# Performance work log

Measured on AMD Instinct MI355X. Metric: run time of the kernel, lower is better.

The kernel has to match this reference:

```python
import jax, jax.numpy as jnp
import numpy as np

B, IMG, P, D, E, K, H = 32, 224, 16, 512, 8, 2, 8
G = IMG // P
T = G * G          # 196 patches
PD = P * P         # 256 patch dim
FF = 4 * D         # expert hidden

def _posenc(t, d):
    pos = jnp.arange(t, dtype=jnp.float32)[:, None]
    i = jnp.arange(0, d, 2, dtype=jnp.float32)
    ang = pos / jnp.power(10000.0, i / d)
    pe = jnp.zeros((t, d), jnp.float32)
    pe = pe.at[:, 0::2].set(jnp.sin(ang))
    pe = pe.at[:, 1::2].set(jnp.cos(ang))
    return pe

def _attn(x, Wq, Wk, Wv, Wo, bo):
    bs, t, d = x.shape
    hs = d // H
    q = (x @ Wq).reshape(bs, t, H, hs).transpose(0, 2, 1, 3)
    k = (x @ Wk).reshape(bs, t, H, hs).transpose(0, 2, 1, 3)
    v = (x @ Wv).reshape(bs, t, H, hs).transpose(0, 2, 1, 3)
    wei = jnp.einsum('bhqd,bhkd->bhqk', q, k) * (hs ** -0.5)
    mask = jnp.tril(jnp.ones((t, t), dtype=bool))
    wei = jax.nn.softmax(jnp.where(mask, wei, -jnp.inf), axis=-1)
    o = jnp.einsum('bhqk,bhkd->bhqd', wei, v).transpose(0, 2, 1, 3).reshape(bs, t, d)
    return o @ Wo + bo

def _router(x, Wt, bt, Wn, bn, noise):
    # NoisyTopkRouter: noisy logits, top-k scatter to -inf background, softmax
    logits = x @ Wt + bt
    noisy = logits + noise * jax.nn.softplus(x @ Wn + bn)
    _, topi = jax.lax.top_k(noisy, K)
    sel = jax.nn.one_hot(topi, E, dtype=jnp.float32).sum(-2) > 0  # [B,T,E] bool
    return jax.nn.softmax(jnp.where(sel, noisy, -jnp.inf), axis=-1)

def _moe(x, gate, Wi, bi, Wo, bo):
    # gate is exactly zero off the top-k set, so dense all-expert compute
    # weighted by gate equals the original masked gather/scatter-add combine.
    h = jax.nn.relu(jnp.einsum('btd,edh->bteh', x, Wi) + bi)
    y = jnp.einsum('bteh,ehd->bted', h, Wo) + bo
    return jnp.einsum('bte,bted->btd', gate, y)

def _ln(x, g, b):
    mu = x.mean(-1, keepdims=True)
    var = ((x - mu) ** 2).mean(-1, keepdims=True)
    return (x - mu) / jnp.sqrt(var + 1e-5) * g + b

def _moe_layer(x, pW, pb, Wq, Wk, Wv, Wo, bo, rtW, rtb, rnW, rnb, eWi, ebi, eWo, ebo, lng, lnb, noise):
    x = x @ pW + pb                       # input_projection
    x = _attn(x, Wq, Wk, Wv, Wo, bo)      # multi-head causal self-attention
    gate = _router(x, rtW, rtb, rnW, rnb, noise)
    y = _moe(x, gate, eWi, ebi, eWo, ebo)
    return _ln(y, lng, lnb)               # dropout is identity in eval

def setup_inputs():
    key = jax.random.key(0)
    shapes = {"x": (B, 1, IMG, IMG), "pemb_W": (PD, D), "pemb_b": (D,), "vec_W": (D, D), "vec_b": (D,), "cls_W": (D, D), "cls_b": (D,)}
    for l in ("1", "2"):
        shapes.update({f"p{l}_W": (D, D), f"p{l}_b": (D,), f"Wq{l}": (D, D), f"Wk{l}": (D, D), f"Wv{l}": (D, D), f"Wo{l}": (D, D), f"bo{l}": (D,), f"rt{l}_W": (D, E), f"rt{l}_b": (E,), f"rn{l}_W": (D, E), f"rn{l}_b": (E,), f"eWi{l}": (E, D, FF), f"ebi{l}": (E, FF), f"eWo{l}": (E, FF, D), f"ebo{l}": (E, D), f"ln{l}_g": (D,), f"ln{l}_b": (D,), f"noise{l}": (B, T, E)})
    out = {}
    for i, (name, shp) in enumerate(shapes.items()):
        k = jax.random.fold_in(key, i)
        if name.startswith("ln") and name.endswith("_g"):
            out[name] = jnp.ones(shp, jnp.float32)
        else:
            scale = 1.0 if name == "x" or name.startswith("noise") else 0.02
            out[name] = jax.random.normal(k, shp, jnp.float32) * scale
    return out

def reference(x, pemb_W, pemb_b, vec_W, vec_b, cls_W, cls_b, p1_W, p1_b, Wq1, Wk1, Wv1, Wo1, bo1, rt1_W, rt1_b, rn1_W, rn1_b, eWi1, ebi1, eWo1, ebo1, ln1_g, ln1_b, noise1, p2_W, p2_b, Wq2, Wk2, Wv2, Wo2, bo2, rt2_W, rt2_b, rn2_W, rn2_b, eWi2, ebi2, eWo2, ebo2, ln2_g, ln2_b, noise2):
    bs = x.shape[0]
    # patchify (c==1): [B,1,IMG,IMG] -> [B,T,PD]
    patches = x[:, 0].reshape(bs, G, P, G, P).transpose(0, 1, 3, 2, 4).reshape(bs, T, PD)
    h = patches @ pemb_W + pemb_b + _posenc(T, D)[None]
    f1 = _moe_layer(h, p1_W, p1_b, Wq1, Wk1, Wv1, Wo1, bo1, rt1_W, rt1_b, rn1_W, rn1_b, eWi1, ebi1, eWo1, ebo1, ln1_g, ln1_b, noise1)
    first_vector = f1 @ vec_W + vec_b
    f2 = _moe_layer(first_vector, p2_W, p2_b, Wq2, Wk2, Wv2, Wo2, bo2, rt2_W, rt2_b, rn2_W, rn2_b, eWi2, ebi2, eWo2, ebo2, ln2_g, ln2_b, noise2)
    second_vector = f2 @ vec_W + vec_b
    # source bug: second_attn_weights is None; treated as uniform ones ->
    # mean over dim1 of ones is 1, so global = sum over patches.
    global_vector = second_vector.sum(axis=1)
    cls_vector = global_vector @ cls_W + cls_b
    return first_vector, second_vector, global_vector, cls_vector
```

## Files before the change

kernel.cpp:

```cpp
#include <hip/hip_runtime.h>

#define BT 6272
#define TT 196
#define DM 512
#define FFD 2048
#define NE 8
#define ABUF 3211264
#define SLOTS 12544

typedef float f32x4 __attribute__((ext_vector_type(4)));
typedef __bf16 bf16x8 __attribute__((ext_vector_type(8)));

__device__ __forceinline__ ushort f2bf(float f){
  union { float f; unsigned u; } v; v.f = f;
  unsigned u = v.u;
  u += 0x7fffu + ((u >> 16) & 1u);
  return (ushort)(u >> 16);
}
__device__ __forceinline__ float bf2f(ushort u){
  union { unsigned u; float f; } c; c.u = ((unsigned)u) << 16; return c.f;
}
__device__ __forceinline__ void splitbf(float v, ushort& hi, ushort& lo){
  union { float f; unsigned u; } c; c.f = v;
  hi = (ushort)(c.u >> 16);
  union { unsigned u; float f; } hf; hf.u = c.u & 0xffff0000u;
  lo = f2bf(v - hf.f);
}
__device__ __forceinline__ void glds16(const ushort* g, ushort* l){
  __builtin_amdgcn_global_load_lds(
      (const __attribute__((address_space(1))) unsigned int*)g,
      (__attribute__((address_space(3))) unsigned int*)l, 16, 0, 0);
}
__device__ __forceinline__ int xcd_swz(int f, int nwg){
  int q = nwg >> 3, r = nwg & 7;
  int xcd = f & 7, i = f >> 3;
  return (xcd < r ? xcd*(q+1) : r*(q+1) + (xcd-r)*q) + i;
}

__global__ void patchify_k(const float* __restrict__ x, ushort* __restrict__ oh, ushort* __restrict__ ol){
  int bt = blockIdx.x;
  int t = bt % TT, b = bt / TT;
  int pd = threadIdx.x;
  int g1 = t / 14, g2 = t % 14, p1 = pd >> 4, p2 = pd & 15;
  int src = (b*224 + g1*16 + p1)*224 + g2*16 + p2;
  float v = x[src];
  ushort hu, lu; splitbf(v, hu, lu);
  oh[(size_t)bt*256 + pd] = hu;
  ol[(size_t)bt*256 + pd] = lu;
}

__global__ void posenc_k(float* __restrict__ pe){
  int t = blockIdx.x, c = threadIdx.x;
  int m2 = c & ~1;
  double ang = (double)t * pow(10000.0, -(double)m2 / 512.0);
  double vv = (c & 1) ? cos(ang) : sin(ang);
  pe[t*DM + c] = (float)vv;
}

__global__ __launch_bounds__(256)
void wsplit_k(const float* __restrict__ src, ushort* __restrict__ dh, ushort* __restrict__ dl,
              int R, int C){
  __shared__ float t[32][33];
  int c0 = blockIdx.x << 5, r0 = blockIdx.y << 5;
  int tx = threadIdx.x & 31, ty = threadIdx.x >> 5;
  #pragma unroll
  for (int i = 0; i < 32; i += 8)
    t[ty+i][tx] = src[(size_t)(r0+ty+i)*C + c0 + tx];
  __syncthreads();
  #pragma unroll
  for (int i = 0; i < 32; i += 8){
    float v = t[tx][ty+i];
    ushort hu, lu; splitbf(v, hu, lu);
    dh[(size_t)(c0+ty+i)*R + r0 + tx] = hu;
    dl[(size_t)(c0+ty+i)*R + r0 + tx] = lu;
  }
}

__global__ __launch_bounds__(256)
void wsplit5e_k(const float* __restrict__ s0, const float* __restrict__ s1,
                const float* __restrict__ s2, const float* __restrict__ s3,
                const float* __restrict__ s4,
                ushort* __restrict__ dQkvH, ushort* __restrict__ dQkvL,
                ushort* __restrict__ dWoH, ushort* __restrict__ dWoL,
                ushort* __restrict__ dPWh, ushort* __restrict__ dPWl)
{
  int z = blockIdx.z;
  int c0 = blockIdx.x << 5, r0 = blockIdx.y << 5;
  int tx = threadIdx.x & 31, ty = threadIdx.x >> 5;
  if (z == 4){
    #pragma unroll
    for (int i = 0; i < 32; i += 8){
      size_t idx = (size_t)(r0+ty+i)*DM + c0 + tx;
      ushort hu, lu; splitbf(s4[idx], hu, lu);
      dPWh[idx] = hu; dPWl[idx] = lu;
    }
    return;
  }
  const float* src = (z==0)? s0 : (z==1)? s1 : (z==2)? s2 : s3;
  ushort* dh; ushort* dl;
  if (z == 3){ dh = dWoH; dl = dWoL; }
  else { dh = dQkvH + (size_t)z*DM*DM; dl = dQkvL + (size_t)z*DM*DM; }
  __shared__ float t[32][33];
  #pragma unroll
  for (int i = 0; i < 32; i += 8)
    t[ty+i][tx] = src[(size_t)(r0+ty+i)*DM + c0 + tx];
  __syncthreads();
  #pragma unroll
  for (int i = 0; i < 32; i += 8){
    float v = t[tx][ty+i];
    ushort hu, lu; splitbf(v, hu, lu);
    dh[(size_t)(c0+ty+i)*DM + r0 + tx] = hu;
    dl[(size_t)(c0+ty+i)*DM + r0 + tx] = lu;
  }
}

__global__ __launch_bounds__(256)
void bfold_k(const float* __restrict__ pb, const float* __restrict__ Wq,
             const float* __restrict__ Wk, const float* __restrict__ Wv,
             float* __restrict__ bf){
  int tid = threadIdx.x;
  int w = tid >> 6, lane = tid & 63;
  int n = blockIdx.x*4 + w;
  const float* W = (n < 512) ? Wq : (n < 1024) ? Wk : Wv;
  int c = n & 511;
  float s = 0.f;
  #pragma unroll
  for (int u = 0; u < 8; ++u){
    int d = (u<<6) + lane;
    s += pb[d] * W[(size_t)d*DM + c];
  }
  #pragma unroll
  for (int off = 32; off; off >>= 1) s += __shfl_xor(s, off, 64);
  if (lane == 0) bf[n] = s;
}

__global__ __launch_bounds__(256)
void gemm_s(const ushort* __restrict__ Ah, const ushort* __restrict__ Al,
            const ushort* __restrict__ Bh, const ushort* __restrict__ Bl,
            const float* __restrict__ bias, const float* __restrict__ pe,
            float* __restrict__ Cf, ushort* __restrict__ Ch, ushort* __restrict__ Cl,
            int N, int kld)
{
  __shared__ __align__(16) ushort smem[4][2*128*32];
  ushort* Ahs = smem[0];
  ushort* Als = smem[1];
  ushort* Bhs = smem[2];
  ushort* Bls = smem[3];
  int gx = gridDim.x, gy = gridDim.y;
  int fblk = blockIdx.x + gx*blockIdx.y;
  int wgt = xcd_swz(fblk, gx*gy);
  int bx = wgt % gx, by = wgt / gx;
  int row0 = by << 7, col0 = bx << 7;
  int tid = threadIdx.x;
  int lane = tid & 63, w = tid >> 6;
  int wr = w >> 1, wc = w & 1;
  int fr = lane & 15, fu = lane >> 4;
  int srow = 16*w + (lane >> 2);
  int cs = ((lane & 3) ^ ((srow >> 1) & 3)) << 3;
  const ushort* gAh0 = Ah + (size_t)(row0 + srow) * kld + cs;
  const ushort* gAh1 = Ah + (size_t)(row0 + 64 + srow) * kld + cs;
  const ushort* gAl0 = Al + (size_t)(row0 + srow) * kld + cs;
  const ushort* gAl1 = Al + (size_t)(row0 + 64 + srow) * kld + cs;
  const ushort* gBh0 = Bh + (size_t)(col0 + srow) * kld + cs;
  const ushort* gBh1 = Bh + (size_t)(col0 + 64 + srow) * kld + cs;
  const ushort* gBl0 = Bl + (size_t)(col0 + srow) * kld + cs;
  const ushort* gBl1 = Bl + (size_t)(col0 + 64 + srow) * kld + cs;
  int lo0 = (16*w)*32, lo1 = (64+16*w)*32;
  #define GSTAGE(koff, nb) { \
    glds16(gAh0 + (koff), &Ahs[(nb)+lo0]); glds16(gAh1 + (koff), &Ahs[(nb)+lo1]); \
    glds16(gAl0 + (koff), &Als[(nb)+lo0]); glds16(gAl1 + (koff), &Als[(nb)+lo1]); \
    glds16(gBh0 + (koff), &Bhs[(nb)+lo0]); glds16(gBh1 + (koff), &Bhs[(nb)+lo1]); \
    glds16(gBl0 + (koff), &Bls[(nb)+lo0]); glds16(gBl1 + (koff), &Bls[(nb)+lo1]); }
  f32x4 acc[4][4] = {};
  int nt = kld >> 5;
  GSTAGE(0, 0)
  GSTAGE(32, 128*32)
  for (int t = 0; t < nt; ++t){
    if (t + 1 < nt) asm volatile("s_waitcnt vmcnt(8)" ::: "memory");
    else            asm volatile("s_waitcnt vmcnt(0)" ::: "memory");
    __builtin_amdgcn_s_barrier();
    asm volatile("" ::: "memory");
    int cb = (t & 1) * (128*32);
    bf16x8 ah[4], al[4];
    #pragma unroll
    for (int i = 0; i < 4; ++i){
      int Ra = (wr<<6) + (i<<4) + fr;
      int oa = cb + Ra*32 + ((fu ^ ((Ra>>1)&3))<<3);
      ah[i] = *(const bf16x8*)&Ahs[oa];
      al[i] = *(const bf16x8*)&Als[oa];
    }
    #pragma unroll
    for (int j = 0; j < 4; ++j){
      int Rb = (wc<<6) + (j<<4) + fr;
      int ob = cb + Rb*32 + ((fu ^ ((Rb>>1)&3))<<3);
      bf16x8 bh = *(const bf16x8*)&Bhs[ob];
      bf16x8 bl = *(const bf16x8*)&Bls[ob];
      #pragma unroll
      for (int i = 0; i < 4; ++i){
        acc[i][j] = __builtin_amdgcn_mfma_f32_16x16x32_bf16(ah[i], bh, acc[i][j], 0, 0, 0);
        acc[i][j] = __builtin_amdgcn_mfma_f32_16x16x32_bf16(al[i], bh, acc[i][j], 0, 0, 0);
        acc[i][j] = __builtin_amdgcn_mfma_f32_16x16x32_bf16(ah[i], bl, acc[i][j], 0, 0, 0);
      }
    }
    asm volatile("" ::: "memory");
    __builtin_amdgcn_s_barrier();
    if (t + 2 < nt) GSTAGE((t+2) << 5, (t & 1) * (128*32))
  }
  #undef GSTAGE
  int fq = lane >> 4;
  if (Cf){
    #pragma unroll
    for (int j = 0; j < 4; ++j){
      int col = col0 + (wc<<6) + (j<<4) + fr;
      float bv = bias ? bias[col] : 0.f;
      #pragma unroll
      for (int i = 0; i < 4; ++i){
        #pragma unroll
        for (int q = 0; q < 4; ++q){
          int rr = row0 + (wr<<6) + (i<<4) + (fq<<2) + q;
          float v = acc[i][j][q] + bv;
          if (pe) v += pe[(size_t)(rr % TT)*DM + col];
          Cf[(size_t)rr*N + col] = v;
        }
      }
    }
  }
  if (Ch){
    ushort* Lh = smem[0];
    ushort* Ll = smem[2];
    __syncthreads();
    #pragma unroll
    for (int j = 0; j < 4; ++j){
      int lcol = (wc<<6) + (j<<4) + fr;
      int col = col0 + lcol;
      float bv = bias ? bias[col] : 0.f;
      #pragma unroll
      for (int i = 0; i < 4; ++i){
        #pragma unroll
        for (int q = 0; q < 4; ++q){
          int lrow = (wr<<6) + (i<<4) + (fq<<2) + q;
          float v = acc[i][j][q] + bv;
          if (pe) v += pe[(size_t)((row0 + lrow) % TT)*DM + col];
          ushort hu, lu; splitbf(v, hu, lu);
          int g = (lrow >> 2) & 7;
          int idx = lrow*128 + ((((lcol>>3) ^ g))<<3) + (lcol & 7);
          Lh[idx] = hu; Ll[idx] = lu;
        }
      }
    }
    __syncthreads();
    #pragma unroll
    for (int pass = 0; pass < 8; ++pass){
      int lrow = pass*16 + (tid >> 4);
      int s = tid & 15;
      int g = (lrow >> 2) & 7;
      int idx = lrow*128 + ((s ^ g)<<3);
      uint4 vh = *(const uint4*)&Lh[idx];
      uint4 vl = *(const uint4*)&Ll[idx];
      size_t off = (size_t)(row0 + lrow)*N + col0 + s*8;
      *(uint4*)&Ch[off] = vh;
      *(uint4*)&Cl[off] = vl;
    }
  }
}

__global__ __launch_bounds__(256)
void gemm_f32(const float* __restrict__ A, const float* __restrict__ Bw,
              float* __restrict__ C, const float* __restrict__ bias,
              float* __restrict__ obf, int M, int N, int K)
{
  __shared__ float As[16][68];
  __shared__ float Bs[16][68];
  int tid = threadIdx.x;
  int row0 = blockIdx.y << 6, col0 = blockIdx.x << 6;
  int ar = tid >> 2, ak = (tid & 3) << 2;
  int bk = tid >> 4, bn = (tid & 15) << 2;
  int n0 = (tid & 15) << 2, m0 = (tid >> 4) << 2;
  float acc[4][4] = {};
  bool arow_ok = (row0 + ar) < M;
  const float* Aldg = A + (size_t)(row0 + ar) * K + ak;
  const float* Bldg = Bw + (size_t)bk * N + col0 + bn;
  for (int k0 = 0; k0 < K; k0 += 16){
    float4 av = make_float4(0.f,0.f,0.f,0.f);
    if (arow_ok) av = *(const float4*)(Aldg + k0);
    float4 bv = *(const float4*)(Bldg + (size_t)k0 * N);
    __syncthreads();
    As[ak+0][ar]=av.x; As[ak+1][ar]=av.y; As[ak+2][ar]=av.z; As[ak+3][ar]=av.w;
    *(float4*)&Bs[bk][bn] = bv;
    __syncthreads();
    #pragma unroll
    for (int kk = 0; kk < 16; ++kk){
      float4 a = *(const float4*)&As[kk][m0];
      float4 b = *(const float4*)&Bs[kk][n0];
      float aa[4] = {a.x,a.y,a.z,a.w};
      float bb[4] = {b.x,b.y,b.z,b.w};
      #pragma unroll
      for (int i = 0; i < 4; ++i)
        #pragma unroll
        for (int j = 0; j < 4; ++j)
          acc[i][j] += aa[i]*bb[j];
    }
  }
  float4 badd = make_float4(0.f,0.f,0.f,0.f);
  if (bias) badd = *(const float4*)(bias + col0 + n0);
  #pragma unroll
  for (int i = 0; i < 4; ++i){
    int gr = row0 + m0 + i;
    if (gr < M){
      float4 r = make_float4(acc[i][0]+badd.x, acc[i][1]+badd.y, acc[i][2]+badd.z, acc[i][3]+badd.w);
      *(float4*)(C + (size_t)gr*N + col0 + n0) = r;
      if (obf) *(float4*)(obf + (size_t)gr*N + col0 + n0) = r;
    }
  }
}

__global__ __launch_bounds__(256)
void fattn_k(const ushort* __restrict__ Xh, const ushort* __restrict__ Xl,
             ushort* __restrict__ oh, ushort* __restrict__ ol)
{
  __shared__ ushort Kh[64][72], Kl[64][72];
  __shared__ ushort Vth[64][72], Vtl[64][72];
  __shared__ ushort Ph[64][72], Pl[64][72];
  int qt = blockIdx.x, bh = blockIdx.y;
  int b = bh >> 3, h = bh & 7;
  int tid = threadIdx.x;
  int w = tid >> 6, lane = tid & 63;
  int fr = lane & 15, fu = lane >> 4;
  int qrow_f = qt*64 + w*16 + fr;
  int qtok = b*TT + (qrow_f < TT ? qrow_f : TT-1);
  const ushort* qph = Xh + (size_t)qtok*1536 + h*64 + fu*8;
  const ushort* qpl = Xl + (size_t)qtok*1536 + h*64 + fu*8;
  bf16x8 qh0 = *(const bf16x8*)(qph);
  bf16x8 qh1 = *(const bf16x8*)(qph + 32);
  bf16x8 ql0 = *(const bf16x8*)(qpl);
  bf16x8 ql1 = *(const bf16x8*)(qpl + 32);
  f32x4 o_acc[4] = {};
  float m_i[4], l_i[4];
  #pragma unroll
  for (int q = 0; q < 4; ++q){ m_i[q] = -3e38f; l_i[q] = 0.f; }
  int sr = tid >> 2, sc = (tid & 3) << 4;
  int ktiles = qt + 1;
  for (int kt = 0; kt < ktiles; ++kt){
    __syncthreads();
    {
      int jrow = kt*64 + sr;
      int jtok = b*TT + (jrow < TT ? jrow : TT-1);
      const ushort* kph = Xh + (size_t)jtok*1536 + 512 + h*64 + sc;
      const ushort* kpl = Xl + (size_t)jtok*1536 + 512 + h*64 + sc;
      *(uint4*)&Kh[sr][sc]   = *(const uint4*)kph;
      *(uint4*)&Kh[sr][sc+8] = *(const uint4*)(kph + 8);
      *(uint4*)&Kl[sr][sc]   = *(const uint4*)kpl;
      *(uint4*)&Kl[sr][sc+8] = *(const uint4*)(kpl + 8);
      const ushort* vph = Xh + (size_t)jtok*1536 + 1024 + h*64 + sc;
      const ushort* vpl = Xl + (size_t)jtok*1536 + 1024 + h*64 + sc;
      ushort tv[16];
      *(uint4*)&tv[0] = *(const uint4*)vph;
      *(uint4*)&tv[8] = *(const uint4*)(vph + 8);
      #pragma unroll
      for (int t = 0; t < 16; ++t) Vth[sc + t][sr] = tv[t];
      *(uint4*)&tv[0] = *(const uint4*)vpl;
      *(uint4*)&tv[8] = *(const uint4*)(vpl + 8);
      #pragma unroll
      for (int t = 0; t < 16; ++t) Vtl[sc + t][sr] = tv[t];
    }
    __syncthreads();
    f32x4 sacc[4] = {};
    #pragma unroll
    for (int j = 0; j < 4; ++j){
      bf16x8 kh0 = *(const bf16x8*)&Kh[j*16 + fr][fu*8];
      bf16x8 kh1 = *(const bf16x8*)&Kh[j*16 + fr][32 + fu*8];
      bf16x8 kl0 = *(const bf16x8*)&Kl[j*16 + fr][fu*8];
      bf16x8 kl1 = *(const bf16x8*)&Kl[j*16 + fr][32 + fu*8];
      sacc[j] = __builtin_amdgcn_mfma_f32_16x16x32_bf16(qh0, kh0, sacc[j], 0, 0, 0);
      sacc[j] = __builtin_amdgcn_mfma_f32_16x16x32_bf16(ql0, kh0, sacc[j], 0, 0, 0);
      sacc[j] = __builtin_amdgcn_mfma_f32_16x16x32_bf16(qh0, kl0, sacc[j], 0, 0, 0);
      sacc[j] = __builtin_amdgcn_mfma_f32_16x16x32_bf16(qh1, kh1, sacc[j], 0, 0, 0);
      sacc[j] = __builtin_amdgcn_mfma_f32_16x16x32_bf16(ql1, kh1, sacc[j], 0, 0, 0);
      sacc[j] = __builtin_amdgcn_mfma_f32_16x16x32_bf16(qh1, kl1, sacc[j], 0, 0, 0);
    }
    int rbase = qt*64 + w*16 + (fu<<2);
    int cg = kt*64 + fr;
    float p[4][4];
    #pragma unroll
    for (int q = 0; q < 4; ++q){
      int rg = rbase + q;
      float sv[4];
      #pragma unroll
      for (int j = 0; j < 4; ++j){
        int cj = cg + j*16;
        sv[j] = (cj <= rg && cj < TT) ? sacc[j][q]*0.125f : -3e38f;
      }
      float mx = fmaxf(fmaxf(sv[0],sv[1]), fmaxf(sv[2],sv[3]));
      #pragma unroll
      for (int off = 1; off < 16; off <<= 1) mx = fmaxf(mx, __shfl_xor(mx, off, 64));
      float mnew = fmaxf(m_i[q], mx);
      float al = expf(m_i[q] - mnew);
      l_i[q] *= al;
      o_acc[0][q] *= al; o_acc[1][q] *= al; o_acc[2][q] *= al; o_acc[3][q] *= al;
      float ps = 0.f;
      #pragma unroll
      for (int j = 0; j < 4; ++j){ p[q][j] = expf(sv[j] - mnew); ps += p[q][j]; }
      #pragma unroll
      for (int off = 1; off < 16; off <<= 1) ps += __shfl_xor(ps, off, 64);
      l_i[q] += ps;
      m_i[q] = mnew;
    }
    #pragma unroll
    for (int q = 0; q < 4; ++q){
      int pr = w*16 + (fu<<2) + q;
      #pragma unroll
      for (int j = 0; j < 4; ++j){
        ushort hu, lu; splitbf(p[q][j], hu, lu);
        Ph[pr][j*16 + fr] = hu;
        Pl[pr][j*16 + fr] = lu;
      }
    }
    bf16x8 ph0 = *(const bf16x8*)&Ph[w*16 + fr][fu*8];
    bf16x8 ph1 = *(const bf16x8*)&Ph[w*16 + fr][32 + fu*8];
    bf16x8 pl0 = *(const bf16x8*)&Pl[w*16 + fr][fu*8];
    bf16x8 pl1 = *(const bf16x8*)&Pl[w*16 + fr][32 + fu*8];
    #pragma unroll
    for (int jd = 0; jd < 4; ++jd){
      bf16x8 vh0 = *(const bf16x8*)&Vth[jd*16 + fr][fu*8];
      bf16x8 vh1 = *(const bf16x8*)&Vth[jd*16 + fr][32 + fu*8];
      bf16x8 vl0 = *(const bf16x8*)&Vtl[jd*16 + fr][fu*8];
      bf16x8 vl1 = *(const bf16x8*)&Vtl[jd*16 + fr][32 + fu*8];
      o_acc[jd] = __builtin_amdgcn_mfma_f32_16x16x32_bf16(ph0, vh0, o_acc[jd], 0, 0, 0);
      o_acc[jd] = __builtin_amdgcn_mfma_f32_16x16x32_bf16(pl0, vh0, o_acc[jd], 0, 0, 0);
      o_acc[jd] = __builtin_amdgcn_mfma_f32_16x16x32_bf16(ph0, vl0, o_acc[jd], 0, 0, 0);
      o_acc[jd] = __builtin_amdgcn_mfma_f32_16x16x32_bf16(ph1, vh1, o_acc[jd], 0, 0, 0);
      o_acc[jd] = __builtin_amdgcn_mfma_f32_16x16x32_bf16(pl1, vh1, o_acc[jd], 0, 0, 0);
      o_acc[jd] = __builtin_amdgcn_mfma_f32_16x16x32_bf16(ph1, vl1, o_acc[jd], 0, 0, 0);
    }
  }
  #pragma unroll
  for (int q = 0; q < 4; ++q){
    int rg = qt*64 + w*16 + (fu<<2) + q;
    if (rg < TT){
      float inv = 1.f / l_i[q];
      size_t rowoff = (size_t)(b*TT + rg)*DM + h*64 + fr;
      #pragma unroll
      for (int jd = 0; jd < 4; ++jd){
        float v = o_acc[jd][q] * inv;
        ushort hu, lu; splitbf(v, hu, lu);
        oh[rowoff + jd*16] = hu;
        ol[rowoff + jd*16] = lu;
      }
    }
  }
}

__global__ __launch_bounds__(256)
void router2_k(const ushort* __restrict__ Xh, const ushort* __restrict__ Xl,
               const float* __restrict__ rtW, const float* __restrict__ rtb,
               const float* __restrict__ rnW, const float* __restrict__ rnb, const float* __restrict__ nz,
               int* __restrict__ tok_e, float* __restrict__ tok_g)
{
  __shared__ float Wt[8*513];
  __shared__ float Wn[8*513];
  int tid = threadIdx.x;
  for (int i = tid*4; i < DM*8; i += 1024){
    float4 t = *(const float4*)(rtW + i);
    float4 n = *(const float4*)(rnW + i);
    int d = i >> 3, e = i & 7;
    Wt[(e+0)*513 + d] = t.x; Wt[(e+1)*513 + d] = t.y; Wt[(e+2)*513 + d] = t.z; Wt[(e+3)*513 + d] = t.w;
    Wn[(e+0)*513 + d] = n.x; Wn[(e+1)*513 + d] = n.y; Wn[(e+2)*513 + d] = n.z; Wn[(e+3)*513 + d] = n.w;
  }
  __syncthreads();
  int w = tid >> 6, lane = tid & 63;
  int t = (blockIdx.x << 2) + w;
  const ushort* xh = Xh + (size_t)t * DM;
  const ushort* xl = Xl + (size_t)t * DM;
  float at[8] = {}, an[8] = {};
  #pragma unroll
  for (int u = 0; u < 8; ++u){
    int d = (u<<6) + lane;
    float xv = bf2f(xh[d]) + bf2f(xl[d]);
    #pragma unroll
    for (int e = 0; e < 8; ++e){
      at[e] += xv * Wt[e*513 + d];
      an[e] += xv * Wn[e*513 + d];
    }
  }
  #pragma unroll
  for (int off = 32; off; off >>= 1){
    #pragma unroll
    for (int e = 0; e < 8; ++e){
      at[e] += __shfl_xor(at[e], off, 64);
      an[e] += __shfl_xor(an[e], off, 64);
    }
  }
  if (lane == 0){
    float ns[8];
    #pragma unroll
    for (int e = 0; e < 8; ++e){
      float lt = at[e] + rtb[e];
      float ln_ = an[e] + rnb[e];
      float sp = (ln_ > 0.f) ? (ln_ + log1pf(expf(-ln_))) : log1pf(expf(ln_));
      ns[e] = lt + nz[(size_t)t*8 + e] * sp;
    }
    int i1 = 0; float n1 = ns[0];
    #pragma unroll
    for (int e = 1; e < 8; ++e) if (ns[e] > n1){ n1 = ns[e]; i1 = e; }
    int i2 = -1; float n2 = -3e38f;
    #pragma unroll
    for (int e = 0; e < 8; ++e) if (e != i1 && ns[e] > n2){ n2 = ns[e]; i2 = e; }
    float ex = expf(n2 - n1);
    float inv = 1.f / (1.f + ex);
    tok_e[t*2]   = i1; tok_g[t*2]   = inv;
    tok_e[t*2+1] = i2; tok_g[t*2+1] = ex * inv;
  }
}

__global__ __launch_bounds__(1024)
void route_assign_k(const int* __restrict__ tok_e, int* __restrict__ offs_g,
                    int* __restrict__ idx_c, int* __restrict__ tok_slot)
{
  __shared__ int hist[NE];
  __shared__ int cur[NE];
  int tid = threadIdx.x;
  int lane = tid & 63;
  if (tid < NE) hist[tid] = 0;
  __syncthreads();
  for (int i = tid; i < BT*2; i += 1024){
    int e = tok_e[i];
    #pragma unroll
    for (int x = 0; x < NE; ++x){
      unsigned long long m = __ballot(e == x);
      if (m && lane == (int)__builtin_ctzll(m)) atomicAdd(&hist[x], __popcll(m));
    }
  }
  __syncthreads();
  if (tid == 0){
    int s = 0;
    for (int e = 0; e < NE; ++e){ offs_g[e] = s; cur[e] = s; s += hist[e]; }
    offs_g[NE] = s;
  }
  __syncthreads();
  for (int i = tid; i < BT*2; i += 1024){
    int e = tok_e[i];
    int p = 0;
    #pragma unroll
    for (int x = 0; x < NE; ++x){
      unsigned long long m = __ballot(e == x);
      if (m){
        int leader = (int)__builtin_ctzll(m);
        int bw = 0;
        if (lane == leader) bw = atomicAdd(&cur[x], __popcll(m));
        bw = __shfl(bw, leader, 64);
        if (e == x) p = bw + __popcll(m & ((lane == 63) ? 0x7fffffffffffffffull : ((1ull << lane) - 1ull)));
      }
    }
    idx_c[p] = i >> 1;
    tok_slot[i] = p;
  }
}

__global__ __launch_bounds__(256)
void transconv2_k(const float* __restrict__ eWi, const float* __restrict__ eWo,
                  ushort* __restrict__ WiT, ushort* __restrict__ WoT){
  __shared__ float t[32][33];
  int z = blockIdx.z;
  const float* src; ushort* dst; int R, C, c0, r0;
  if (z < NE){
    src = eWi + (size_t)z*DM*FFD; dst = WiT + (size_t)z*DM*FFD;
    R = DM; C = FFD; c0 = blockIdx.x << 5; r0 = blockIdx.y << 5;
  } else {
    int e = z - NE;
    src = eWo + (size_t)e*FFD*DM; dst = WoT + (size_t)e*FFD*DM;
    R = FFD; C = DM; c0 = blockIdx.y << 5; r0 = blockIdx.x << 5;
  }
  int tx = threadIdx.x & 31, ty = threadIdx.x >> 5;
  #pragma unroll
  for (int i = 0; i < 32; i += 8)
    t[ty+i][tx] = src[(size_t)(r0+ty+i)*C + c0 + tx];
  __syncthreads();
  #pragma unroll
  for (int i = 0; i < 32; i += 8)
    dst[(size_t)(c0+ty+i)*R + r0 + tx] = f2bf(t[tx][ty+i]);
}

template<int MODE>
__global__ __launch_bounds__(256)
void moe_mfma(const ushort* __restrict__ A, const int* __restrict__ aidx,
              const ushort* __restrict__ Bt,
              const float* __restrict__ bias, const int* __restrict__ offs,
              void* __restrict__ Out, int kld, int ldb, int out_ld, int accum)
{
  __shared__ __align__(16) ushort smem[2][2*128*32];
  ushort* As = smem[0];
  ushort* Bs = smem[1];
  int gx = gridDim.x, gy = gridDim.y;
  int nwg = gx * gy * (int)gridDim.z;
  int fblk = blockIdx.x + gx*(blockIdx.y + gy*blockIdx.z);
  int wgt = xcd_swz(fblk, nwg);
  int bx = wgt % gx; wgt /= gx;
  int by = wgt % gy; int bz = wgt / gy;
  int e = bz;
  int base = offs[e], cnt = offs[e+1] - base;
  int row0 = by << 7;
  if (row0 >= cnt) return;
  int col0 = bx << 7;
  int tid = threadIdx.x, lane = tid & 63, w = tid >> 6;
  int wr = w >> 1, wc = w & 1;
  int fr = lane & 15, fu = lane >> 4;
  int srow = 16*w + (lane >> 2);
  int cs = ((lane & 3) ^ ((srow >> 1) & 3)) << 3;
  int s0 = base + row0 + srow;      if (s0 > SLOTS-1) s0 = SLOTS-1;
  int s1 = base + row0 + 64 + srow; if (s1 > SLOTS-1) s1 = SLOTS-1;
  int r0i = (MODE == 0) ? aidx[s0] : s0;
  int r1i = (MODE == 0) ? aidx[s1] : s1;
  const ushort* gA0 = A + (size_t)r0i * kld + cs;
  const ushort* gA1 = A + (size_t)r1i * kld + cs;
  const ushort* Bb = Bt + (size_t)e * ((size_t)FFD*DM);
  const ushort* gB0 = Bb + (size_t)(col0 + srow) * ldb + cs;
  const ushort* gB1 = Bb + (size_t)(col0 + 64 + srow) * ldb + cs;
  int lo0 = (16*w)*32, lo1 = (64+16*w)*32;
  #define MSTAGE(koff, nb) { \
    glds16(gA0 + (koff), &As[(nb)+lo0]); glds16(gA1 + (koff), &As[(nb)+lo1]); \
    glds16(gB0 + (koff), &Bs[(nb)+lo0]); glds16(gB1 + (koff), &Bs[(nb)+lo1]); }
  f32x4 acc[4][4] = {};
  int nt = kld >> 5;
  MSTAGE(0, 0)
  MSTAGE(32, 128*32)
  for (int t = 0; t < nt; ++t){
    if (t + 1 < nt) asm volatile("s_waitcnt vmcnt(4)" ::: "memory");
    else            asm volatile("s_waitcnt vmcnt(0)" ::: "memory");
    __builtin_amdgcn_s_barrier();
    asm volatile("" ::: "memory");
    int cb = (t & 1) * (128*32);
    bf16x8 af[4], bf[4];
    #pragma unroll
    for (int i = 0; i < 4; ++i){
      int Ra = (wr<<6) + (i<<4) + fr;
      af[i] = *(const bf16x8*)&As[cb + Ra*32 + ((fu ^ ((Ra>>1)&3))<<3)];
      int Rb = (wc<<6) + (i<<4) + fr;
      bf[i] = *(const bf16x8*)&Bs[cb + Rb*32 + ((fu ^ ((Rb>>1)&3))<<3)];
    }
    #pragma unroll
    for (int i = 0; i < 4; ++i)
      #pragma unroll
      for (int j = 0; j < 4; ++j)
        acc[i][j] = __builtin_amdgcn_mfma_f32_16x16x32_bf16(af[i], bf[j], acc[i][j], 0, 0, 0);
    asm volatile("" ::: "memory");
    __builtin_amdgcn_s_barrier();
    if (t + 2 < nt) MSTAGE((t+2) << 5, (t & 1) * (128*32))
  }
  #undef MSTAGE
  int fq = lane >> 4;
  if (MODE == 0){
    ushort* Ls = smem[0];
    __syncthreads();
    #pragma unroll
    for (int j = 0; j < 4; ++j){
      int lcol = (wc<<6) + (j<<4) + fr;
      float bv = bias[(size_t)e*FFD + col0 + lcol];
      #pragma unroll
      for (int i = 0; i < 4; ++i){
        #pragma unroll
        for (int q = 0; q < 4; ++q){
          int lrow = (wr<<6) + (i<<4) + (fq<<2) + q;
          float vv = acc[i][j][q] + bv;
          int g = (lrow >> 2) & 7;
          Ls[lrow*128 + ((((lcol>>3) ^ g))<<3) + (lcol & 7)] = f2bf(fmaxf(vv, 0.f));
        }
      }
    }
    __syncthreads();
    #pragma unroll
    for (int pass = 0; pass < 8; ++pass){
      int lrow = pass*16 + (tid >> 4);
      int s = tid & 15;
      int g = (lrow >> 2) & 7;
      uint4 v = *(const uint4*)&Ls[lrow*128 + ((s ^ g)<<3)];
      int gr = row0 + lrow;
      if (gr < cnt)
        *(uint4*)&((ushort*)Out)[(size_t)(base+gr)*out_ld + col0 + s*8] = v;
    }
  } else {
    #pragma unroll
    for (int j = 0; j < 4; ++j){
      int col = col0 + (wc<<6) + (j<<4) + fr;
      float bv = bias[(size_t)e*DM + col];
      #pragma unroll
      for (int i = 0; i < 4; ++i){
        #pragma unroll
        for (int q = 0; q < 4; ++q){
          int rr = row0 + (wr<<6) + (i<<4) + (fq<<2) + q;
          if (rr < cnt){
            float* yp = (float*)Out + (size_t)(base+rr)*out_ld + col;
            *yp = acc[i][j][q] + (accum ? *yp : bv);
          }
        }
      }
    }
  }
}

__global__ __launch_bounds__(256)
void combine_ln_k(const float* __restrict__ Ye, const int* __restrict__ tok_slot,
                  const float* __restrict__ tok_g, const float* __restrict__ g,
                  const float* __restrict__ bb, ushort* __restrict__ oh, ushort* __restrict__ ol)
{
  int t = blockIdx.x, tid = threadIdx.x;
  int s1 = tok_slot[t*2], s2 = tok_slot[t*2+1];
  float g1 = tok_g[t*2], g2 = tok_g[t*2+1];
  const float* y1 = Ye + (size_t)s1*DM;
  const float* y2 = Ye + (size_t)s2*DM;
  float v0 = g1*y1[tid]     + g2*y2[tid];
  float v1 = g1*y1[tid+256] + g2*y2[tid+256];
  __shared__ float red[8];
  int w = tid >> 6, lane = tid & 63;
  float s = v0 + v1;
  #pragma unroll
  for (int off = 32; off; off >>= 1) s += __shfl_xor(s, off, 64);
  if (lane == 0) red[w] = s;
  __syncthreads();
  float mu = (red[0]+red[1]+red[2]+red[3]) * (1.f/512.f);
  float d0 = v0 - mu, d1 = v1 - mu;
  float q2 = d0*d0 + d1*d1;
  #pragma unroll
  for (int off = 32; off; off >>= 1) q2 += __shfl_xor(q2, off, 64);
  if (lane == 0) red[4+w] = q2;
  __syncthreads();
  float var = (red[4]+red[5]+red[6]+red[7]) * (1.f/512.f);
  float r = 1.f / sqrtf(var + 1e-5f);
  float r0v = d0*r*g[tid]     + bb[tid];
  float r1v = d1*r*g[tid+256] + bb[tid+256];
  ushort hu, lu;
  splitbf(r0v, hu, lu);
  oh[(size_t)t*DM + tid] = hu; ol[(size_t)t*DM + tid] = lu;
  splitbf(r1v, hu, lu);
  oh[(size_t)t*DM + tid + 256] = hu; ol[(size_t)t*DM + tid + 256] = lu;
}

__global__ void gsum_k(const float* __restrict__ sv, float* __restrict__ gb, float* __restrict__ gout){
  int i = blockIdx.x*256 + threadIdx.x;
  int b = i >> 9, d = i & 511;
  const float* p = sv + (size_t)b*TT*DM + d;
  float s = 0.f;
  for (int t = 0; t < TT; ++t) s += p[(size_t)t*DM];
  gb[i] = s; gout[i] = s;
}

extern "C" void kernel_launch(void* const* d_in, const int* in_sizes, int n_in,
                              void* d_out, int out_size, void* d_ws, size_t ws_size,
                              hipStream_t stream)
{
  (void)in_sizes; (void)n_in; (void)out_size;
  const float* xin   = (const float*)d_in[0];
  const float* pembW = (const float*)d_in[1];
  const float* pembB = (const float*)d_in[2];
  const float* vecW  = (const float*)d_in[3];
  const float* vecB  = (const float*)d_in[4];
  const float* clsW  = (const float*)d_in[5];
  const float* clsB  = (const float*)d_in[6];
  float* out = (float*)d_out;

  const size_t QKV_SH  = (size_t)2*BT*1536;
  const size_t RMIN_SH = QKV_SH + (size_t)2*1536*DM + (size_t)2*DM*DM;
  const size_t FIXF =
      (size_t)SLOTS*DM
    + (size_t)2*ABUF
    + (size_t)NE*FFD*DM
    + (size_t)256*DM
    + (size_t)DM*DM
    + (size_t)3*DM*DM
    + (size_t)DM*DM
    + (size_t)TT*DM + 2048
    + 16384*2 + SLOTS + SLOTS*3 + 64;
  int fcw = 256;
  for (int cand = 2048; cand >= 256; cand >>= 1){
    size_t reg_sh = (size_t)SLOTS*cand > RMIN_SH ? (size_t)SLOTS*cand : RMIN_SH;
    size_t need = (FIXF + reg_sh/2) * sizeof(float);
    if (need <= ws_size){ fcw = cand; break; }
  }
  size_t region_sh = (size_t)SLOTS*fcw > RMIN_SH ? (size_t)SLOTS*fcw : RMIN_SH;

  float* ws = (float*)d_ws;
  float* Yexp = ws;
  ushort* S0h = (ushort*)(Yexp + (size_t)SLOTS*DM);
  ushort* S0l = S0h + ABUF;
  ushort* S1h = S0l + ABUF;
  ushort* S1l = S1h + ABUF;
  ushort* region = S1l + ABUF;
  ushort* WiT  = region + region_sh;
  ushort* WoT  = WiT + (size_t)NE*FFD*DM;
  ushort* PembH = WoT + (size_t)NE*FFD*DM;
  ushort* PembL = PembH + 256*DM;
  ushort* VecH = PembL + 256*DM;
  ushort* VecL = VecH + DM*DM;
  ushort* QkvWH = VecL + DM*DM;
  ushort* QkvWL = QkvWH + 3*DM*DM;
  ushort* WoSH = QkvWL + 3*DM*DM;
  ushort* WoSL = WoSH + DM*DM;
  float* pe    = (float*)(WoSL + DM*DM);
  float* bfold = pe + TT*DM;
  float* gbv   = bfold + 2048;
  float* clsbuf= gbv + 16384;
  float* tok_g = clsbuf + 16384;
  int* tok_e   = (int*)(tok_g + SLOTS);
  int* tok_slot= tok_e + SLOTS;
  int* idx_c   = tok_slot + SLOTS;
  int* offs    = idx_c + SLOTS;
  ushort* QKVh = region;
  ushort* QKVl = region + (size_t)BT*1536;
  ushort* FoldWH = region + QKV_SH;
  ushort* FoldWL = FoldWH + (size_t)1536*DM;
  ushort* PWh  = FoldWL + (size_t)1536*DM;
  ushort* PWl  = PWh + (size_t)DM*DM;
  ushort* H1b  = region;
  ushort* PATh = region;
  ushort* PATl = region + (size_t)BT*256;

  patchify_k<<<dim3(BT), dim3(256), 0, stream>>>(xin, PATh, PATl);
  posenc_k<<<dim3(TT), dim3(512), 0, stream>>>(pe);
  wsplit_k<<<dim3(16, 8), dim3(256), 0, stream>>>(pembW, PembH, PembL, 256, DM);
  wsplit_k<<<dim3(16, 16), dim3(256), 0, stream>>>(vecW, VecH, VecL, DM, DM);
  gemm_s<<<dim3(4,49), dim3(256), 0, stream>>>(PATh, PATl, PembH, PembL, pembB, pe,
                                               nullptr, S0h, S0l, DM, 256);

  ushort *INh = S0h, *INl = S0l, *TPh = S1h, *TPl = S1l;
  for (int l = 0; l < 2; ++l){
    int base = 7 + 18*l;
    const float* pW  = (const float*)d_in[base+0];
    const float* pb  = (const float*)d_in[base+1];
    const float* Wq  = (const float*)d_in[base+2];
    const float* Wk  = (const float*)d_in[base+3];
    const float* Wv  = (const float*)d_in[base+4];
    const float* Wo  = (const float*)d_in[base+5];
    const float* bo  = (const float*)d_in[base+6];
    const float* rtW = (const float*)d_in[base+7];
    const float* rtb = (const float*)d_in[base+8];
    const float* rnW = (const float*)d_in[base+9];
    const float* rnb = (const float*)d_in[base+10];
    const float* eWi = (const float*)d_in[base+11];
    const float* ebi = (const float*)d_in[base+12];
    const float* eWo = (const float*)d_in[base+13];
    const float* ebo = (const float*)d_in[base+14];
    const float* lng = (const float*)d_in[base+15];
    const float* lnb = (const float*)d_in[base+16];
    const float* nz  = (const float*)d_in[base+17];

    wsplit5e_k<<<dim3(16,16,5), dim3(256), 0, stream>>>(Wq, Wk, Wv, Wo, pW,
                                                        QkvWH, QkvWL, WoSH, WoSL, PWh, PWl);
    gemm_s<<<dim3(4,12), dim3(256), 0, stream>>>(QkvWH, QkvWL, PWh, PWl, nullptr, nullptr,
                                                 nullptr, FoldWH, FoldWL, DM, DM);
    bfold_k<<<dim3(384), dim3(256), 0, stream>>>(pb, Wq, Wk, Wv, bfold);
    gemm_s<<<dim3(12,49), dim3(256), 0, stream>>>(INh, INl, FoldWH, FoldWL, bfold, nullptr,
                                                 nullptr, QKVh, QKVl, 1536, DM);
    fattn_k<<<dim3(4,256), dim3(256), 0, stream>>>(QKVh, QKVl, INh, INl);
    gemm_s<<<dim3(4,49), dim3(256), 0, stream>>>(INh, INl, WoSH, WoSL, bo, nullptr,
                                                 nullptr, TPh, TPl, DM, DM);
    transconv2_k<<<dim3(64, 16, 2*NE), dim3(256), 0, stream>>>(eWi, eWo, WiT, WoT);
    router2_k<<<dim3(BT/4), dim3(256), 0, stream>>>(TPh, TPl, rtW, rtb, rnW, rnb, nz, tok_e, tok_g);
    route_assign_k<<<dim3(1), dim3(1024), 0, stream>>>(tok_e, offs, idx_c, tok_slot);
    for (int c0 = 0; c0 < FFD; c0 += fcw){
      moe_mfma<0><<<dim3(fcw/128, 49, NE), dim3(256), 0, stream>>>(
          TPh, idx_c, WiT + (size_t)c0*DM, ebi + c0, offs, (void*)H1b, DM, DM, fcw, 0);
      moe_mfma<1><<<dim3(DM/128, 49, NE), dim3(256), 0, stream>>>(
          H1b, nullptr, WoT + c0, ebo, offs, (void*)Yexp, fcw, FFD, DM, c0);
    }
    combine_ln_k<<<dim3(BT), dim3(256), 0, stream>>>(Yexp, tok_slot, tok_g, lng, lnb, INh, INl);
    gemm_s<<<dim3(4,49), dim3(256), 0, stream>>>(INh, INl, VecH, VecL, vecB, nullptr,
                                                 out + (size_t)l*ABUF, TPh, TPl, DM, DM);
    ushort* th = INh; INh = TPh; TPh = th;
    ushort* tl = INl; INl = TPl; TPl = tl;
  }

  gsum_k<<<dim3(64), dim3(256), 0, stream>>>(out + ABUF, gbv, out + 2*ABUF);
  gemm_f32<<<dim3(8,1), dim3(256), 0, stream>>>(gbv, clsW, clsbuf, clsB, out + 2*ABUF + 16384, 32, DM, DM);
}
```

Before: 942.4 us.

## Compact MoE tile grid via tile map and triple-buffer GEMM K-loop

The routing kernel now builds a compact list of (expert, row-block) tiles, so the expert GEMMs launch over at most 112 row tiles instead of 49×8 mostly-empty blocks that would exit early. Empty launch slots cost less and the XCD swizzle spreads only real tiles. The MFMA K-loop moves from two LDS buffers to three, and the next stage is issued right after the barrier, which removes the second barrier per iteration. This triples A/B LDS use per block (48KB), which may lower occupancy.

```diff
diff --git a/kernel.cpp b/kernel.cpp
--- a/kernel.cpp
+++ b/kernel.cpp
@@ -7,6 +7,7 @@
 #define NE 8
 #define ABUF 3211264
 #define SLOTS 12544
+#define MAXTILES 112
 
 typedef float f32x4 __attribute__((ext_vector_type(4)));
 typedef __bf16 bf16x8 __attribute__((ext_vector_type(8)));
@@ -514,7 +515,8 @@
 
 __global__ __launch_bounds__(1024)
 void route_assign_k(const int* __restrict__ tok_e, int* __restrict__ offs_g,
-                    int* __restrict__ idx_c, int* __restrict__ tok_slot)
+                    int* __restrict__ idx_c, int* __restrict__ tok_slot,
+                    int* __restrict__ tmap)
 {
   __shared__ int hist[NE];
   __shared__ int cur[NE];
@@ -535,6 +537,12 @@
     int s = 0;
     for (int e = 0; e < NE; ++e){ offs_g[e] = s; cur[e] = s; s += hist[e]; }
     offs_g[NE] = s;
+    int tt = 0;
+    for (int e = 0; e < NE; ++e){
+      int nb = (hist[e] + 127) >> 7;
+      for (int b = 0; b < nb; ++b) tmap[tt++] = (e << 16) | b;
+    }
+    for (; tt < MAXTILES; ++tt) tmap[tt] = -1;
   }
   __syncthreads();
   for (int i = tid; i < BT*2; i += 1024){
@@ -585,21 +593,22 @@
 void moe_mfma(const ushort* __restrict__ A, const int* __restrict__ aidx,
               const ushort* __restrict__ Bt,
               const float* __restrict__ bias, const int* __restrict__ offs,
+              const int* __restrict__ tmap,
               void* __restrict__ Out, int kld, int ldb, int out_ld, int accum)
 {
-  __shared__ __align__(16) ushort smem[2][2*128*32];
-  ushort* As = smem[0];
-  ushort* Bs = smem[1];
+  __shared__ __align__(16) ushort smem[6*128*32];
+  const int TB = 128*32;
+  ushort* As = smem;
+  ushort* Bs = smem + 3*TB;
   int gx = gridDim.x, gy = gridDim.y;
-  int nwg = gx * gy * (int)gridDim.z;
-  int fblk = blockIdx.x + gx*(blockIdx.y + gy*blockIdx.z);
-  int wgt = xcd_swz(fblk, nwg);
-  int bx = wgt % gx; wgt /= gx;
-  int by = wgt % gy; int bz = wgt / gy;
-  int e = bz;
+  int fblk = blockIdx.x + gx*blockIdx.y;
+  int wgt = xcd_swz(fblk, gx*gy);
+  int bx = wgt % gx, ty = wgt / gx;
+  int tm = tmap[ty];
+  if (tm < 0) return;
+  int e = tm >> 16;
   int base = offs[e], cnt = offs[e+1] - base;
-  int row0 = by << 7;
-  if (row0 >= cnt) return;
+  int row0 = (tm & 0xffff) << 7;
   int col0 = bx << 7;
   int tid = threadIdx.x, lane = tid & 63, w = tid >> 6;
   int wr = w >> 1, wc = w & 1;
@@ -616,19 +625,20 @@
   const ushort* gB0 = Bb + (size_t)(col0 + srow) * ldb + cs;
   const ushort* gB1 = Bb + (size_t)(col0 + 64 + srow) * ldb + cs;
   int lo0 = (16*w)*32, lo1 = (64+16*w)*32;
-  #define MSTAGE(koff, nb) { \
-    glds16(gA0 + (koff), &As[(nb)+lo0]); glds16(gA1 + (koff), &As[(nb)+lo1]); \
-    glds16(gB0 + (koff), &Bs[(nb)+lo0]); glds16(gB1 + (koff), &Bs[(nb)+lo1]); }
+  #define MSTAGE(koff, b) { \
+    glds16(gA0 + (koff), &As[(b)*TB+lo0]); glds16(gA1 + (koff), &As[(b)*TB+lo1]); \
+    glds16(gB0 + (koff), &Bs[(b)*TB+lo0]); glds16(gB1 + (koff), &Bs[(b)*TB+lo1]); }
   f32x4 acc[4][4] = {};
   int nt = kld >> 5;
   MSTAGE(0, 0)
-  MSTAGE(32, 128*32)
+  MSTAGE(32, 1)
   for (int t = 0; t < nt; ++t){
     if (t + 1 < nt) asm volatile("s_waitcnt vmcnt(4)" ::: "memory");
     else            asm volatile("s_waitcnt vmcnt(0)" ::: "memory");
     __builtin_amdgcn_s_barrier();
     asm volatile("" ::: "memory");
-    int cb = (t & 1) * (128*32);
+    if (t + 2 < nt) MSTAGE((t+2) << 5, (t+2)%3)
+    int cb = (t%3) * TB;
     bf16x8 af[4], bf[4];
     #pragma unroll
     for (int i = 0; i < 4; ++i){
@@ -643,13 +653,11 @@
       for (int j = 0; j < 4; ++j)
         acc[i][j] = __builtin_amdgcn_mfma_f32_16x16x32_bf16(af[i], bf[j], acc[i][j], 0, 0, 0);
     asm volatile("" ::: "memory");
-    __builtin_amdgcn_s_barrier();
-    if (t + 2 < nt) MSTAGE((t+2) << 5, (t & 1) * (128*32))
   }
   #undef MSTAGE
   int fq = lane >> 4;
   if (MODE == 0){
-    ushort* Ls = smem[0];
+    ushort* Ls = smem;
     __syncthreads();
     #pragma unroll
     for (int j = 0; j < 4; ++j){
@@ -768,7 +776,7 @@
     + (size_t)3*DM*DM
     + (size_t)DM*DM
     + (size_t)TT*DM + 2048
-    + 16384*2 + SLOTS + SLOTS*3 + 64;
+    + 16384*2 + SLOTS + SLOTS*3 + 256;
   int fcw = 256;
   for (int cand = 2048; cand >= 256; cand >>= 1){
     size_t reg_sh = (size_t)SLOTS*cand > RMIN_SH ? (size_t)SLOTS*cand : RMIN_SH;
@@ -803,6 +811,7 @@
   int* tok_slot= tok_e + SLOTS;
   int* idx_c   = tok_slot + SLOTS;
   int* offs    = idx_c + SLOTS;
+  int* tmap    = offs + 16;
   ushort* QKVh = region;
   ushort* QKVl = region + (size_t)BT*1536;
   ushort* FoldWH = region + QKV_SH;
@@ -854,12 +863,12 @@
                                                  nullptr, TPh, TPl, DM, DM);
     transconv2_k<<<dim3(64, 16, 2*NE), dim3(256), 0, stream>>>(eWi, eWo, WiT, WoT);
     router2_k<<<dim3(BT/4), dim3(256), 0, stream>>>(TPh, TPl, rtW, rtb, rnW, rnb, nz, tok_e, tok_g);
-    route_assign_k<<<dim3(1), dim3(1024), 0, stream>>>(tok_e, offs, idx_c, tok_slot);
+    route_assign_k<<<dim3(1), dim3(1024), 0, stream>>>(tok_e, offs, idx_c, tok_slot, tmap);
     for (int c0 = 0; c0 < FFD; c0 += fcw){
-      moe_mfma<0><<<dim3(fcw/128, 49, NE), dim3(256), 0, stream>>>(
-          TPh, idx_c, WiT + (size_t)c0*DM, ebi + c0, offs, (void*)H1b, DM, DM, fcw, 0);
-      moe_mfma<1><<<dim3(DM/128, 49, NE), dim3(256), 0, stream>>>(
-          H1b, nullptr, WoT + c0, ebo, offs, (void*)Yexp, fcw, FFD, DM, c0);
+      moe_mfma<0><<<dim3(fcw/128, MAXTILES), dim3(256), 0, stream>>>(
+          TPh, idx_c, WiT + (size_t)c0*DM, ebi + c0, offs, tmap, (void*)H1b, DM, DM, fcw, 0);
+      moe_mfma<1><<<dim3(DM/128, MAXTILES), dim3(256), 0, stream>>>(
+          H1b, nullptr, WoT + c0, ebo, offs, tmap, (void*)Yexp, fcw, FFD, DM, c0);
     }
     combine_ln_k<<<dim3(BT), dim3(256), 0, stream>>>(Yexp, tok_slot, tok_g, lng, lnb, INh, INl);
     gemm_s<<<dim3(4,49), dim3(256), 0, stream>>>(INh, INl, VecH, VecL, vecB, nullptr,
```

Result: no change. 954.0 us (+1.2%).

## Split-K the MoE down-projection into two partial buffers and swizzle attention blocks

Applied to the files above, without the earlier changes.

When the workspace is large enough, the expert FFN runs as one full-width up-projection launch plus one down-projection launch. The down-projection splits K into two halves written to separate fp32 buffers, and the combine+LayerNorm kernel sums the two partials. This doubles the down-proj grid, which is meant to improve CU occupancy and remove the chunked launch loop with its read-modify-write accumulation. It costs an extra SLOTS×DM fp32 buffer and extra reads in combine. Flash-attention blocks are also remapped with the XCD swizzle to improve L2 locality.

```diff
diff --git a/kernel.cpp b/kernel.cpp
--- a/kernel.cpp
+++ b/kernel.cpp
@@ -321,7 +321,9 @@
   __shared__ ushort Kh[64][72], Kl[64][72];
   __shared__ ushort Vth[64][72], Vtl[64][72];
   __shared__ ushort Ph[64][72], Pl[64][72];
-  int qt = blockIdx.x, bh = blockIdx.y;
+  int flat = blockIdx.x + (blockIdx.y << 2);
+  int wgt = xcd_swz(flat, 4*256);
+  int qt = wgt & 3, bh = wgt >> 2;
   int b = bh >> 3, h = bh & 7;
   int tid = threadIdx.x;
   int w = tid >> 6, lane = tid & 63;
@@ -585,7 +587,8 @@
 void moe_mfma(const ushort* __restrict__ A, const int* __restrict__ aidx,
               const ushort* __restrict__ Bt,
               const float* __restrict__ bias, const int* __restrict__ offs,
-              void* __restrict__ Out, int kld, int ldb, int out_ld, int accum)
+              void* __restrict__ Out, int kld, int ldb, int out_ld,
+              int klen, int accum, int nks)
 {
   __shared__ __align__(16) ushort smem[2][2*128*32];
   ushort* As = smem[0];
@@ -596,11 +599,14 @@
   int wgt = xcd_swz(fblk, nwg);
   int bx = wgt % gx; wgt /= gx;
   int by = wgt % gy; int bz = wgt / gy;
+  int kh = 0;
+  if (MODE == 1 && nks == 2){ kh = bx >> 2; bx &= 3; }
   int e = bz;
   int base = offs[e], cnt = offs[e+1] - base;
   int row0 = by << 7;
   if (row0 >= cnt) return;
   int col0 = bx << 7;
+  size_t kofs = (size_t)kh * klen;
   int tid = threadIdx.x, lane = tid & 63, w = tid >> 6;
   int wr = w >> 1, wc = w & 1;
   int fr = lane & 15, fu = lane >> 4;
@@ -610,17 +616,17 @@
   int s1 = base + row0 + 64 + srow; if (s1 > SLOTS-1) s1 = SLOTS-1;
   int r0i = (MODE == 0) ? aidx[s0] : s0;
   int r1i = (MODE == 0) ? aidx[s1] : s1;
-  const ushort* gA0 = A + (size_t)r0i * kld + cs;
-  const ushort* gA1 = A + (size_t)r1i * kld + cs;
+  const ushort* gA0 = A + (size_t)r0i * kld + kofs + cs;
+  const ushort* gA1 = A + (size_t)r1i * kld + kofs + cs;
   const ushort* Bb = Bt + (size_t)e * ((size_t)FFD*DM);
-  const ushort* gB0 = Bb + (size_t)(col0 + srow) * ldb + cs;
-  const ushort* gB1 = Bb + (size_t)(col0 + 64 + srow) * ldb + cs;
+  const ushort* gB0 = Bb + (size_t)(col0 + srow) * ldb + kofs + cs;
+  const ushort* gB1 = Bb + (size_t)(col0 + 64 + srow) * ldb + kofs + cs;
   int lo0 = (16*w)*32, lo1 = (64+16*w)*32;
   #define MSTAGE(koff, nb) { \
     glds16(gA0 + (koff), &As[(nb)+lo0]); glds16(gA1 + (koff), &As[(nb)+lo1]); \
     glds16(gB0 + (koff), &Bs[(nb)+lo0]); glds16(gB1 + (koff), &Bs[(nb)+lo1]); }
   f32x4 acc[4][4] = {};
-  int nt = kld >> 5;
+  int nt = klen >> 5;
   MSTAGE(0, 0)
   MSTAGE(32, 128*32)
   for (int t = 0; t < nt; ++t){
@@ -678,18 +684,20 @@
         *(uint4*)&((ushort*)Out)[(size_t)(base+gr)*out_ld + col0 + s*8] = v;
     }
   } else {
+    float* Yb = (float*)Out + (size_t)kh * ((size_t)SLOTS * DM);
     #pragma unroll
     for (int j = 0; j < 4; ++j){
       int col = col0 + (wc<<6) + (j<<4) + fr;
-      float bv = bias[(size_t)e*DM + col];
+      float bv = (kh == 0) ? bias[(size_t)e*DM + col] : 0.f;
       #pragma unroll
       for (int i = 0; i < 4; ++i){
         #pragma unroll
         for (int q = 0; q < 4; ++q){
           int rr = row0 + (wr<<6) + (i<<4) + (fq<<2) + q;
           if (rr < cnt){
-            float* yp = (float*)Out + (size_t)(base+rr)*out_ld + col;
-            *yp = acc[i][j][q] + (accum ? *yp : bv);
+            float* yp = Yb + (size_t)(base+rr)*out_ld + col;
+            if (nks == 2) *yp = acc[i][j][q] + bv;
+            else          *yp = acc[i][j][q] + (accum ? *yp : bv);
           }
         }
       }
@@ -698,7 +706,8 @@
 }
 
 __global__ __launch_bounds__(256)
-void combine_ln_k(const float* __restrict__ Ye, const int* __restrict__ tok_slot,
+void combine_ln_k(const float* __restrict__ Ye, const float* __restrict__ Ye2,
+                  const int* __restrict__ tok_slot,
                   const float* __restrict__ tok_g, const float* __restrict__ g,
                   const float* __restrict__ bb, ushort* __restrict__ oh, ushort* __restrict__ ol)
 {
@@ -707,8 +716,16 @@
   float g1 = tok_g[t*2], g2 = tok_g[t*2+1];
   const float* y1 = Ye + (size_t)s1*DM;
   const float* y2 = Ye + (size_t)s2*DM;
-  float v0 = g1*y1[tid]     + g2*y2[tid];
-  float v1 = g1*y1[tid+256] + g2*y2[tid+256];
+  float a0 = y1[tid],      a1 = y1[tid+256];
+  float b0 = y2[tid],      b1 = y2[tid+256];
+  if (Ye2){
+    const float* z1 = Ye2 + (size_t)s1*DM;
+    const float* z2 = Ye2 + (size_t)s2*DM;
+    a0 += z1[tid]; a1 += z1[tid+256];
+    b0 += z2[tid]; b1 += z2[tid+256];
+  }
+  float v0 = g1*a0 + g2*b0;
+  float v1 = g1*a1 + g2*b1;
   __shared__ float red[8];
   int w = tid >> 6, lane = tid & 63;
   float s = v0 + v1;
@@ -768,18 +785,27 @@
     + (size_t)3*DM*DM
     + (size_t)DM*DM
     + (size_t)TT*DM + 2048
-    + 16384*2 + SLOTS + SLOTS*3 + 64;
-  int fcw = 256;
-  for (int cand = 2048; cand >= 256; cand >>= 1){
-    size_t reg_sh = (size_t)SLOTS*cand > RMIN_SH ? (size_t)SLOTS*cand : RMIN_SH;
-    size_t need = (FIXF + reg_sh/2) * sizeof(float);
-    if (need <= ws_size){ fcw = cand; break; }
+    + 16384*2 + SLOTS + SLOTS*3 + 256;
+  int fcw = 256, ksplit = 1;
+  {
+    size_t reg_sh = (size_t)SLOTS*2048 > RMIN_SH ? (size_t)SLOTS*2048 : RMIN_SH;
+    size_t need2 = (FIXF + (size_t)SLOTS*DM + reg_sh/2) * sizeof(float);
+    if (need2 <= ws_size){ ksplit = 2; fcw = 2048; }
+    else {
+      for (int cand = 2048; cand >= 256; cand >>= 1){
+        size_t rs = (size_t)SLOTS*cand > RMIN_SH ? (size_t)SLOTS*cand : RMIN_SH;
+        size_t need = (FIXF + rs/2) * sizeof(float);
+        if (need <= ws_size){ fcw = cand; break; }
+      }
+    }
   }
   size_t region_sh = (size_t)SLOTS*fcw > RMIN_SH ? (size_t)SLOTS*fcw : RMIN_SH;
+  size_t yex2f = (ksplit == 2) ? (size_t)SLOTS*DM : 0;
 
   float* ws = (float*)d_ws;
-  float* Yexp = ws;
-  ushort* S0h = (ushort*)(Yexp + (size_t)SLOTS*DM);
+  float* Yexp  = ws;
+  float* Yexp2 = ws + (size_t)SLOTS*DM;
+  ushort* S0h = (ushort*)(Yexp + (size_t)SLOTS*DM + yex2f);
   ushort* S0l = S0h + ABUF;
   ushort* S1h = S0l + ABUF;
   ushort* S1l = S1h + ABUF;
@@ -855,13 +881,21 @@
     transconv2_k<<<dim3(64, 16, 2*NE), dim3(256), 0, stream>>>(eWi, eWo, WiT, WoT);
     router2_k<<<dim3(BT/4), dim3(256), 0, stream>>>(TPh, TPl, rtW, rtb, rnW, rnb, nz, tok_e, tok_g);
     route_assign_k<<<dim3(1), dim3(1024), 0, stream>>>(tok_e, offs, idx_c, tok_slot);
-    for (int c0 = 0; c0 < FFD; c0 += fcw){
-      moe_mfma<0><<<dim3(fcw/128, 49, NE), dim3(256), 0, stream>>>(
-          TPh, idx_c, WiT + (size_t)c0*DM, ebi + c0, offs, (void*)H1b, DM, DM, fcw, 0);
-      moe_mfma<1><<<dim3(DM/128, 49, NE), dim3(256), 0, stream>>>(
-          H1b, nullptr, WoT + c0, ebo, offs, (void*)Yexp, fcw, FFD, DM, c0);
-    }
-    combine_ln_k<<<dim3(BT), dim3(256), 0, stream>>>(Yexp, tok_slot, tok_g, lng, lnb, INh, INl);
+    if (ksplit == 2){
+      moe_mfma<0><<<dim3(16, 49, NE), dim3(256), 0, stream>>>(
+          TPh, idx_c, WiT, ebi, offs, (void*)H1b, DM, DM, 2048, 512, 0, 1);
+      moe_mfma<1><<<dim3(8, 49, NE), dim3(256), 0, stream>>>(
+          H1b, nullptr, WoT, ebo, offs, (void*)Yexp, 2048, FFD, DM, 1024, 0, 2);
+    } else {
+      for (int c0 = 0; c0 < FFD; c0 += fcw){
+        moe_mfma<0><<<dim3(fcw/128, 49, NE), dim3(256), 0, stream>>>(
+            TPh, idx_c, WiT + (size_t)c0*DM, ebi + c0, offs, (void*)H1b, DM, DM, fcw, 512, 0, 1);
+        moe_mfma<1><<<dim3(DM/128, 49, NE), dim3(256), 0, stream>>>(
+            H1b, nullptr, WoT + c0, ebo, offs, (void*)Yexp, fcw, FFD, DM, fcw, c0, 1);
+      }
+    }
+    combine_ln_k<<<dim3(BT), dim3(256), 0, stream>>>(Yexp, (ksplit == 2) ? Yexp2 : nullptr,
+                                                     tok_slot, tok_g, lng, lnb, INh, INl);
     gemm_s<<<dim3(4,49), dim3(256), 0, stream>>>(INh, INl, VecH, VecL, vecB, nullptr,
                                                  out + (size_t)l*ABUF, TPh, TPl, DM, DM);
     ushort* th = INh; INh = TPh; TPh = th;
```

New measurement: 959.9 us. Within noise of the previous version (+1.9%).
